# Kernel optimization log

Measured on AMD Instinct MI355X. Metric: run time of the kernel, lower is better.

## Reference

```python
import jax, jax.numpy as jnp
import numpy as np

MASK_ID = -100
L, D, HID, NH = 10, 768, 3072, 12
DH = D // NH
REACH = 2  # (sliding_window_size - 1) // 2 with window 5


def _layernorm(x, g, b, eps=1e-5):
    mu = x.mean(-1, keepdims=True)
    var = ((x - mu) ** 2).mean(-1, keepdims=True)
    return (x - mu) * jax.lax.rsqrt(var + eps) * g + b


def _adaln(x, temb, w, bb, g, be):
    # AdaLayerNormShiftScale: linear(silu(temb)) -> (scale, shift)
    e = jax.nn.silu(temb) @ w + bb
    scale, shift = jnp.split(e, 2, axis=-1)
    return _layernorm(x, g, be) * (1.0 + scale) + shift


def _timestep_emb(t):
    half = D // 2
    exponent = -np.log(10000.0) * jnp.arange(half, dtype=jnp.float32) / (half - 1.0)
    freq = jnp.exp(exponent)  # [half]
    emb = t.astype(jnp.float32)[..., None] * freq  # [b,s,half]
    return jnp.concatenate([jnp.sin(emb), jnp.cos(emb)], axis=-1)  # [b,s,D]


def setup_inputs():
    key = jax.random.key(0)
    ks = jax.random.split(key, 16)
    b, s = 4, 1024
    # packed token ids: 4 samples of 256 tokens (16x16 grid), last 64 tokens padding
    idx = np.arange(s)
    sid = idx // 256
    hpos = (idx % 256) // 16
    wpos = idx % 16
    sid = np.where(idx >= 960, MASK_ID, sid)
    tok = np.stack([sid, hpos, wpos], axis=-1)  # [s,3]
    token_ids = jnp.asarray(np.broadcast_to(tok, (b, s, 3)).copy(), dtype=jnp.int32)
    t = jax.random.randint(ks[0], (b, 1), 0, L + 1).astype(jnp.int32)
    t = jnp.broadcast_to(t, (b, s))

    def w(k, shape):
        return jax.random.normal(k, shape, jnp.float32) * 0.02

    return dict(
        x=jax.random.normal(ks[1], (b, s, D), jnp.float32),
        t=t,
        token_ids=token_ids,
        proj_in_w=w(ks[2], (D, D)), proj_in_b=jnp.zeros((D,), jnp.float32),
        h_emb=w(ks[3], (64, D)), w_emb=w(ks[4], (64, D)),
        adaln1_w=w(ks[5], (L, D, 2 * D)), adaln1_b=jnp.zeros((L, 2 * D), jnp.float32),
        ln1_g=jnp.ones((L, D), jnp.float32), ln1_b=jnp.zeros((L, D), jnp.float32),
        qkv_w=w(ks[6], (L, D, 3 * D)), qkv_b=jnp.zeros((L, 3 * D), jnp.float32),
        o_w=w(ks[7], (L, D, D)), o_b=jnp.zeros((L, D), jnp.float32),
        adaln2_w=w(ks[8], (L, D, 2 * D)), adaln2_b=jnp.zeros((L, 2 * D), jnp.float32),
        ln2_g=jnp.ones((L, D), jnp.float32), ln2_b=jnp.zeros((L, D), jnp.float32),
        fc1_w=w(ks[9], (L, D, HID)), fc1_b=jnp.zeros((L, HID), jnp.float32),
        fc2_w=w(ks[10], (L, HID, D)), fc2_b=jnp.zeros((L, D), jnp.float32),
        nout_w=w(ks[11], (D, 2 * D)), nout_b=jnp.zeros((2 * D,), jnp.float32),
        nout_g=jnp.ones((D,), jnp.float32), nout_beta=jnp.zeros((D,), jnp.float32),
    )


def _encoder(x, t, token_ids, proj_in_w, proj_in_b, h_emb, w_emb,
             adaln1_w, adaln1_b, ln1_g, ln1_b, qkv_w, qkv_b, o_w, o_b,
             adaln2_w, adaln2_b, ln2_g, ln2_b, fc1_w, fc1_b, fc2_w, fc2_b,
             nout_w, nout_b, nout_g, nout_beta):
    b, s, _ = x.shape
    sample_ids = token_ids[..., 0]          # [b,s]
    pos = token_ids[..., 1:]                # [b,s,2]
    x = x @ proj_in_w + proj_in_b
    x = x + h_emb[pos[..., 0]] + w_emb[pos[..., 1]]

    # block-sparse mask: same packed sample, Chebyshev sliding window, no padding queries
    same = sample_ids[:, :, None] == sample_ids[:, None, :]              # [b,s,s]
    cheby = jnp.abs(pos[:, :, None, :] - pos[:, None, :, :]).max(-1)      # [b,s,s]
    notpad_q = (sample_ids != MASK_ID)[:, :, None]
    mask = same & (cheby <= REACH) & notpad_q                             # [b,s,s]
    row_valid = mask.any(-1)[..., None]                                   # [b,s,1]

    temb = _timestep_emb(t)  # [b,s,D]
    scale = 1.0 / np.sqrt(DH)
    for i in range(L):
        h1 = _adaln(x, temb, adaln1_w[i], adaln1_b[i], ln1_g[i], ln1_b[i])
        qkv = h1 @ qkv_w[i] + qkv_b[i]
        q, k, v = jnp.split(qkv, 3, axis=-1)
        q = q.reshape(b, s, NH, DH)
        k = k.reshape(b, s, NH, DH)
        v = v.reshape(b, s, NH, DH)
        scores = jnp.einsum('bqhd,bkhd->bhqk', q, k) * scale
        scores = jnp.where(mask[:, None], scores, -1e30)
        attn = jax.nn.softmax(scores, axis=-1)
        o = jnp.einsum('bhqk,bkhd->bqhd', attn, v).reshape(b, s, D)
        o = jnp.where(row_valid, o, 0.0)  # fully-masked (padding) rows -> 0
        x = x + o @ o_w[i] + o_b[i]
        h2 = _adaln(x, temb, adaln2_w[i], adaln2_b[i], ln2_g[i], ln2_b[i])
        x = x + jax.nn.gelu(h2 @ fc1_w[i] + fc1_b[i], approximate=False) @ fc2_w[i] + fc2_b[i]
    x = _adaln(x, temb, nout_w, nout_b, nout_g, nout_beta)
    return x


def reference(x, t, token_ids, proj_in_w, proj_in_b, h_emb, w_emb,
              adaln1_w, adaln1_b, ln1_g, ln1_b, qkv_w, qkv_b, o_w, o_b,
              adaln2_w, adaln2_b, ln2_g, ln2_b, fc1_w, fc1_b, fc2_w, fc2_b,
              nout_w, nout_b, nout_g, nout_beta):
    return _encoder(x, t, token_ids, proj_in_w, proj_in_b, h_emb, w_emb,
                    adaln1_w, adaln1_b, ln1_g, ln1_b, qkv_w, qkv_b, o_w, o_b,
                    adaln2_w, adaln2_b, ln2_g, ln2_b, fc1_w, fc1_b, fc2_w, fc2_b,
                    nout_w, nout_b, nout_g, nout_beta)
```

## Files before the change

kernel.cpp:

```cpp
#include <hip/hip_runtime.h>
#include <hip/hip_bf16.h>
#include <math.h>

#define MASK_ID (-100)
#define SEQ 1024
#define BATCH 4
#define DMODEL 768
#define NHEAD 12
#define DHEAD 64
#define NLAYER 10
#define HIDDEN 3072

typedef unsigned short ushort_t;
typedef unsigned int uint_t;

__device__ __forceinline__ ushort_t f2bf(float f) {
    uint_t u = __float_as_uint(f);
    u = u + 0x7fffu + ((u >> 16) & 1u);
    return (ushort_t)(u >> 16);
}
__device__ __forceinline__ float bf2f(ushort_t u) {
    return __uint_as_float(((uint_t)u) << 16);
}

__device__ __forceinline__ void async_ld16(ushort_t* lds, const ushort_t* g) {
    __builtin_amdgcn_global_load_lds((__attribute__((address_space(1))) const void*)g,
                                     (__attribute__((address_space(3))) void*)lds, 16, 0, 0);
}

#define WAITVM(n) asm volatile("s_waitcnt vmcnt(" #n ")" ::: "memory")

__global__ void temb_silu_kernel(const int* __restrict__ t, float* __restrict__ stemb) {
    int b = blockIdx.x;
    int j = threadIdx.x;
    float tv = (float)t[b * SEQ];
    float freq = expf(-logf(10000.f) * (float)j / 383.f);
    float arg = tv * freq;
    float s = sinf(arg), c = cosf(arg);
    stemb[b * DMODEL + j]       = s / (1.f + expf(-s));
    stemb[b * DMODEL + 384 + j] = c / (1.f + expf(-c));
}

__global__ __launch_bounds__(256)
void adaln_partial_kernel(const float* __restrict__ stemb,
                          const float* __restrict__ a1w,
                          const float* __restrict__ a2w,
                          const float* __restrict__ nw,
                          float* __restrict__ partial) {
    int chunk = blockIdx.x;
    int kc    = blockIdx.y;
    int slot  = blockIdx.z;
    int tid = threadIdx.x;
    int col = chunk * 256 + tid;
    const float* W;
    if (slot == 20) W = nw;
    else {
        int i = slot >> 1;
        W = ((slot & 1) ? a2w : a1w) + (size_t)i * DMODEL * 2 * DMODEL;
    }
    __shared__ float sb[4 * 96];
    for (int idx = tid; idx < 4 * 96; idx += 256) {
        int bb = idx / 96, kk = idx % 96;
        sb[idx] = stemb[bb * DMODEL + kc * 96 + kk];
    }
    __syncthreads();
    const float* Wp = W + (size_t)(kc * 96) * (2 * DMODEL) + col;
    float a0 = 0.f, a1 = 0.f, a2 = 0.f, a3 = 0.f;
    #pragma unroll 4
    for (int kk = 0; kk < 96; ++kk) {
        float w = Wp[(size_t)kk * (2 * DMODEL)];
        a0 = fmaf(sb[kk], w, a0);
        a1 = fmaf(sb[96 + kk], w, a1);
        a2 = fmaf(sb[192 + kk], w, a2);
        a3 = fmaf(sb[288 + kk], w, a3);
    }
    size_t base = ((size_t)(slot * 8 + kc) * 4) * (2 * DMODEL) + col;
    partial[base + 0 * 2 * DMODEL] = a0;
    partial[base + 1 * 2 * DMODEL] = a1;
    partial[base + 2 * 2 * DMODEL] = a2;
    partial[base + 3 * 2 * DMODEL] = a3;
}

__global__ __launch_bounds__(256)
void adaln_reduce_kernel(const float* __restrict__ partial,
                         const float* __restrict__ a1b, const float* __restrict__ a2b,
                         const float* __restrict__ nb,
                         float* __restrict__ e_all) {
    int chunk = blockIdx.x;
    int slot  = blockIdx.y;
    int col = chunk * 256 + threadIdx.x;
    const float* bb;
    if (slot == 20) bb = nb;
    else {
        int i = slot >> 1;
        bb = ((slot & 1) ? a2b : a1b) + i * 2 * DMODEL;
    }
    float bias = bb[col];
    float s0 = bias, s1 = bias, s2 = bias, s3 = bias;
    #pragma unroll
    for (int kc = 0; kc < 8; ++kc) {
        size_t base = ((size_t)(slot * 8 + kc) * 4) * (2 * DMODEL) + col;
        s0 += partial[base + 0 * 2 * DMODEL];
        s1 += partial[base + 1 * 2 * DMODEL];
        s2 += partial[base + 2 * 2 * DMODEL];
        s3 += partial[base + 3 * 2 * DMODEL];
    }
    size_t o = (size_t)slot * 4 * (2 * DMODEL) + col;
    e_all[o + 0 * 2 * DMODEL] = s0;
    e_all[o + 1 * 2 * DMODEL] = s1;
    e_all[o + 2 * 2 * DMODEL] = s2;
    e_all[o + 3 * 2 * DMODEL] = s3;
}

__global__ __launch_bounds__(256)
void transpose_bf16_kernel(const float* __restrict__ in, ushort_t* __restrict__ out,
                           int R, int C) {
    __shared__ float tile[32][33];
    int tx = threadIdx.x & 31, ty = threadIdx.x >> 5;
    int c0 = blockIdx.x * 32, r0 = blockIdx.y * 32;
    #pragma unroll
    for (int i = 0; i < 4; ++i)
        tile[ty + 8 * i][tx] = in[(size_t)(r0 + ty + 8 * i) * C + c0 + tx];
    __syncthreads();
    #pragma unroll
    for (int i = 0; i < 4; ++i)
        out[(size_t)(c0 + ty + 8 * i) * R + r0 + tx] = f2bf(tile[tx][ty + 8 * i]);
}

__global__ __launch_bounds__(256)
void transpose_all_kernel(const float* __restrict__ w0, const float* __restrict__ w1,
                          const float* __restrict__ w2, const float* __restrict__ w3,
                          ushort_t* __restrict__ o0, ushort_t* __restrict__ o1,
                          ushort_t* __restrict__ o2, ushort_t* __restrict__ o3) {
    int layer = blockIdx.y;
    int id = blockIdx.x;
    const float* in; ushort_t* out; int R, C, tile_id, TX;
    if (id < 216) {
        in = w0 + (size_t)layer * DMODEL * 3 * DMODEL; out = o0 + (size_t)layer * 3 * DMODEL * DMODEL;
        R = DMODEL; C = 3 * DMODEL; tile_id = id; TX = 36;
    } else if (id < 288) {
        in = w1 + (size_t)layer * DMODEL * DMODEL; out = o1 + (size_t)layer * DMODEL * DMODEL;
        R = DMODEL; C = DMODEL; tile_id = id - 216; TX = 12;
    } else if (id < 576) {
        in = w2 + (size_t)layer * DMODEL * HIDDEN; out = o2 + (size_t)layer * HIDDEN * DMODEL;
        R = DMODEL; C = HIDDEN; tile_id = id - 288; TX = 48;
    } else {
        in = w3 + (size_t)layer * HIDDEN * DMODEL; out = o3 + (size_t)layer * DMODEL * HIDDEN;
        R = HIDDEN; C = DMODEL; tile_id = id - 576; TX = 12;
    }
    int c0 = (tile_id % TX) * 64, r0 = (tile_id / TX) * 128;
    __shared__ float tl[128][65];
    int tid = threadIdx.x;
    #pragma unroll
    for (int i = 0; i < 32; ++i) {
        int idx = i * 256 + tid;
        int r = idx >> 6, c = idx & 63;
        tl[r][c] = in[(size_t)(r0 + r) * C + c0 + c];
    }
    __syncthreads();
    #pragma unroll
    for (int j = 0; j < 16; ++j) {
        int idx = j * 256 + tid;
        int oc = idx >> 6, pr = idx & 63;
        float a = tl[pr * 2][oc], b = tl[pr * 2 + 1][oc];
        uint_t pk = (uint_t)f2bf(a) | ((uint_t)f2bf(b) << 16);
        *(uint_t*)&out[(size_t)(c0 + oc) * R + r0 + pr * 2] = pk;
    }
}

__global__ __launch_bounds__(256)
void f32_to_bf16_kernel(const float* __restrict__ in, ushort_t* __restrict__ out, int n8) {
    int i = blockIdx.x * 256 + threadIdx.x;
    if (i >= n8) return;
    float4 a = ((const float4*)in)[2 * i];
    float4 b = ((const float4*)in)[2 * i + 1];
    uint4 o;
    o.x = (uint_t)f2bf(a.x) | ((uint_t)f2bf(a.y) << 16);
    o.y = (uint_t)f2bf(a.z) | ((uint_t)f2bf(a.w) << 16);
    o.z = (uint_t)f2bf(b.x) | ((uint_t)f2bf(b.y) << 16);
    o.w = (uint_t)f2bf(b.z) | ((uint_t)f2bf(b.w) << 16);
    ((uint4*)out)[i] = o;
}

template<int OUT_BF>
__global__ __launch_bounds__(256)
void ln_adaln_kernel(const float* __restrict__ in, void* __restrict__ outv,
                     const float* __restrict__ g, const float* __restrict__ be,
                     const float* __restrict__ e) {
    int wid = threadIdx.x >> 6, lane = threadIdx.x & 63;
    int row = blockIdx.x * 4 + wid;
    int b = row >> 10;
    const float* xr = in + (size_t)row * DMODEL;
    float v[12];
    float s = 0.f, ss = 0.f;
    #pragma unroll
    for (int j = 0; j < 12; ++j) {
        v[j] = xr[lane + j * 64];
        s += v[j];
        ss = fmaf(v[j], v[j], ss);
    }
    #pragma unroll
    for (int o = 1; o < 64; o <<= 1) { s += __shfl_xor(s, o); ss += __shfl_xor(ss, o); }
    float mu = s * (1.f / DMODEL);
    float var = ss * (1.f / DMODEL) - mu * mu;
    float rs = rsqrtf(var + 1e-5f);
    const float* esc = e + (size_t)b * (2 * DMODEL);
    #pragma unroll
    for (int j = 0; j < 12; ++j) {
        int c = lane + j * 64;
        float y = (v[j] - mu) * rs * g[c] + be[c];
        y = y * (1.f + esc[c]) + esc[DMODEL + c];
        if (OUT_BF) ((ushort_t*)outv)[(size_t)row * DMODEL + c] = f2bf(y);
        else        ((float*)outv)[(size_t)row * DMODEL + c] = y;
    }
}

__device__ __forceinline__ float gelu_exact(float x) {
    return 0.5f * x * (1.f + erff(x * 0.70710678118654752f));
}

template<int BM, int BN, int EPI, int OCC>
__global__ __launch_bounds__(256, OCC)
void gemm_bf16(const ushort_t* __restrict__ A, const ushort_t* __restrict__ Wt,
               const float* __restrict__ bias, void* __restrict__ outv,
               const float* __restrict__ emb_h, const float* __restrict__ emb_w,
               const int* __restrict__ tok,
               int M, int N, int K) {
    constexpr int WM = BM / 2, WN = BN / 2;
    constexpr int FM = WM / 16, FN = WN / 16;
    constexpr int BUF = (BM + BN) * 64;
    constexpr int LPT = (BM + BN) / 32;
    using f32x4  = __attribute__((ext_vector_type(4))) float;
    using bf16x8 = __attribute__((ext_vector_type(8))) short;

    __shared__ __align__(16) ushort_t lds[3 * BUF];

    int tid = threadIdx.x;
    int lane = tid & 63, wid = tid >> 6;
    int wr = wid >> 1, wc = wid & 1;
    int l16 = lane & 15, lg = lane >> 4;
    int sw = l16 & 7;

    int nx = N / BN;
    int cpx = gridDim.x >> 3;
    int wg = blockIdx.x;
    int wgid = (wg & 7) * cpx + (wg >> 3);
    int bx = wgid % nx, by = wgid / nx;
    int bm0 = by * BM, bn0 = bx * BN;

    f32x4 acc[FM][FN];
    #pragma unroll
    for (int m = 0; m < FM; ++m)
        #pragma unroll
        for (int n = 0; n < FN; ++n)
            #pragma unroll
            for (int r = 0; r < 4; ++r) acc[m][n][r] = 0.f;

    const ushort_t* Abase = A + (size_t)bm0 * K;
    const ushort_t* Bbase = Wt + (size_t)bn0 * K;

    #define STAGE(bufi, kt)                                                             \
        do {                                                                            \
            _Pragma("unroll")                                                           \
            for (int s2 = 0; s2 < BM / 32; ++s2) {                                      \
                int ca = s2 * 256 + tid;                                                \
                int rw = ca >> 3, kcs = (ca & 7) ^ (rw & 7);                            \
                async_ld16(&lds[(bufi) * BUF + ca * 8],                                 \
                           Abase + (size_t)rw * K + (kt) * 64 + kcs * 8);               \
            }                                                                           \
            _Pragma("unroll")                                                           \
            for (int s2 = 0; s2 < BN / 32; ++s2) {                                      \
                int ca = s2 * 256 + tid;                                                \
                int rw = ca >> 3, kcs = (ca & 7) ^ (rw & 7);                            \
                async_ld16(&lds[(bufi) * BUF + BM * 64 + ca * 8],                       \
                           Bbase + (size_t)rw * K + (kt) * 64 + kcs * 8);               \
            }                                                                           \
        } while (0)

    int nk = K >> 6;
    STAGE(0, 0);
    STAGE(1, 1);
    int bufi = 0;
    for (int kt = 0; kt < nk; ++kt) {
        int nxt = bufi + 2; if (nxt >= 3) nxt -= 3;
        if (kt + 2 < nk) {
            STAGE(nxt, kt + 2);
            if constexpr (LPT == 4) WAITVM(8); else WAITVM(12);
        } else if (kt + 1 < nk) {
            if constexpr (LPT == 4) WAITVM(4); else WAITVM(6);
        } else {
            WAITVM(0);
        }
        __builtin_amdgcn_s_barrier();
        __builtin_amdgcn_s_setprio(1);
        #pragma unroll
        for (int kk = 0; kk < 2; ++kk) {
            bf16x8 af[FM], bfr[FN];
            #pragma unroll
            for (int m = 0; m < FM; ++m) {
                int row = wr * WM + m * 16 + l16;
                int csw = (kk * 4 + lg) ^ sw;
                af[m] = *(const bf16x8*)&lds[bufi * BUF + row * 64 + csw * 8];
            }
            #pragma unroll
            for (int n = 0; n < FN; ++n) {
                int row = wc * WN + n * 16 + l16;
                int csw = (kk * 4 + lg) ^ sw;
                bfr[n] = *(const bf16x8*)&lds[bufi * BUF + BM * 64 + row * 64 + csw * 8];
            }
            #pragma unroll
            for (int m = 0; m < FM; ++m)
                #pragma unroll
                for (int n = 0; n < FN; ++n)
                    acc[m][n] = __builtin_amdgcn_mfma_f32_16x16x32_bf16(af[m], bfr[n], acc[m][n], 0, 0, 0);
        }
        __builtin_amdgcn_s_setprio(0);
        __builtin_amdgcn_s_barrier();
        ++bufi; if (bufi >= 3) bufi = 0;
    }
    #undef STAGE

    int r0 = bm0 + wr * WM, c0 = bn0 + wc * WN;
    #pragma unroll
    for (int m = 0; m < FM; ++m) {
        #pragma unroll
        for (int n = 0; n < FN; ++n) {
            int cc = c0 + n * 16 + l16;
            float bcol = bias[cc];
            #pragma unroll
            for (int r = 0; r < 4; ++r) {
                int row = r0 + m * 16 + lg * 4 + r;
                float v = acc[m][n][r] + bcol;
                if (EPI == 0) {
                    ((ushort_t*)outv)[(size_t)row * N + cc] = f2bf(v);
                } else if (EPI == 1) {
                    int p0 = tok[row * 3 + 1], p1 = tok[row * 3 + 2];
                    v += emb_h[p0 * DMODEL + cc] + emb_w[p1 * DMODEL + cc];
                    ((float*)outv)[(size_t)row * N + cc] = v;
                } else if (EPI == 2) {
                    float* op = (float*)outv + (size_t)row * N + cc;
                    *op = *op + v;
                } else {
                    ((ushort_t*)outv)[(size_t)row * N + cc] = f2bf(gelu_exact(v));
                }
            }
        }
    }
}

__global__ __launch_bounds__(256)
void attn_kernel(const ushort_t* __restrict__ qkv, const int* __restrict__ tok,
                 ushort_t* __restrict__ o_out) {
    int tid = threadIdx.x;
    int u = tid >> 2, part = tid & 3;
    int q = blockIdx.x * 16 + (u & 15);
    int h = blockIdx.y * 4 + (u >> 4);
    int b = blockIdx.z;
    int m = b * SEQ + q;
    ushort_t* op = o_out + (size_t)m * DMODEL + h * DHEAD + part * 16;
    int sid = tok[m * 3];
    if (sid == MASK_ID) {
        uint4 z = {0u, 0u, 0u, 0u};
        ((uint4*)op)[0] = z;
        ((uint4*)op)[1] = z;
        return;
    }
    int qh = tok[m * 3 + 1], qw = tok[m * 3 + 2];
    const ushort_t* qp = qkv + (size_t)m * (3 * DMODEL) + h * DHEAD + part * 16;
    float qv[16], ov[16];
    {
        uint4 u0 = ((const uint4*)qp)[0];
        uint4 u1 = ((const uint4*)qp)[1];
        qv[0] = bf2f(u0.x & 0xffff); qv[1] = bf2f(u0.x >> 16);
        qv[2] = bf2f(u0.y & 0xffff); qv[3] = bf2f(u0.y >> 16);
        qv[4] = bf2f(u0.z & 0xffff); qv[5] = bf2f(u0.z >> 16);
        qv[6] = bf2f(u0.w & 0xffff); qv[7] = bf2f(u0.w >> 16);
        qv[8]  = bf2f(u1.x & 0xffff); qv[9]  = bf2f(u1.x >> 16);
        qv[10] = bf2f(u1.y & 0xffff); qv[11] = bf2f(u1.y >> 16);
        qv[12] = bf2f(u1.z & 0xffff); qv[13] = bf2f(u1.z >> 16);
        qv[14] = bf2f(u1.w & 0xffff); qv[15] = bf2f(u1.w >> 16);
    }
    #pragma unroll
    for (int i = 0; i < 16; ++i) ov[i] = 0.f;
    float mx = -1e30f, den = 0.f;
    for (int dh = -2; dh <= 2; ++dh) {
        for (int dw = -2; dw <= 2; ++dw) {
            int kq = q + dh * 16 + dw;
            if (kq < 0 || kq >= SEQ) continue;
            int km = b * SEQ + kq;
            if (tok[km * 3] != sid) continue;
            int kh2 = tok[km * 3 + 1], kw2 = tok[km * 3 + 2];
            int adh = kh2 - qh; if (adh < 0) adh = -adh;
            int adw = kw2 - qw; if (adw < 0) adw = -adw;
            if (adh > 2 || adw > 2) continue;
            const ushort_t* kp = qkv + (size_t)km * (3 * DMODEL) + DMODEL + h * DHEAD + part * 16;
            float dot;
            {
                uint4 u0 = ((const uint4*)kp)[0];
                uint4 u1 = ((const uint4*)kp)[1];
                dot = qv[0] * bf2f(u0.x & 0xffff);
                dot = fmaf(qv[1], bf2f(u0.x >> 16), dot);
                dot = fmaf(qv[2], bf2f(u0.y & 0xffff), dot);
                dot = fmaf(qv[3], bf2f(u0.y >> 16), dot);
                dot = fmaf(qv[4], bf2f(u0.z & 0xffff), dot);
                dot = fmaf(qv[5], bf2f(u0.z >> 16), dot);
                dot = fmaf(qv[6], bf2f(u0.w & 0xffff), dot);
                dot = fmaf(qv[7], bf2f(u0.w >> 16), dot);
                dot = fmaf(qv[8],  bf2f(u1.x & 0xffff), dot);
                dot = fmaf(qv[9],  bf2f(u1.x >> 16), dot);
                dot = fmaf(qv[10], bf2f(u1.y & 0xffff), dot);
                dot = fmaf(qv[11], bf2f(u1.y >> 16), dot);
                dot = fmaf(qv[12], bf2f(u1.z & 0xffff), dot);
                dot = fmaf(qv[13], bf2f(u1.z >> 16), dot);
                dot = fmaf(qv[14], bf2f(u1.w & 0xffff), dot);
                dot = fmaf(qv[15], bf2f(u1.w >> 16), dot);
            }
            dot += __shfl_xor(dot, 1);
            dot += __shfl_xor(dot, 2);
            float sc = dot * 0.125f;
            float nm = fmaxf(mx, sc);
            float c1 = expf(mx - nm);
            float c2 = expf(sc - nm);
            den = den * c1 + c2;
            const ushort_t* vp = qkv + (size_t)km * (3 * DMODEL) + 2 * DMODEL + h * DHEAD + part * 16;
            {
                uint4 u0 = ((const uint4*)vp)[0];
                uint4 u1 = ((const uint4*)vp)[1];
                ov[0] = ov[0] * c1 + c2 * bf2f(u0.x & 0xffff);
                ov[1] = ov[1] * c1 + c2 * bf2f(u0.x >> 16);
                ov[2] = ov[2] * c1 + c2 * bf2f(u0.y & 0xffff);
                ov[3] = ov[3] * c1 + c2 * bf2f(u0.y >> 16);
                ov[4] = ov[4] * c1 + c2 * bf2f(u0.z & 0xffff);
                ov[5] = ov[5] * c1 + c2 * bf2f(u0.z >> 16);
                ov[6] = ov[6] * c1 + c2 * bf2f(u0.w & 0xffff);
                ov[7] = ov[7] * c1 + c2 * bf2f(u0.w >> 16);
                ov[8]  = ov[8]  * c1 + c2 * bf2f(u1.x & 0xffff);
                ov[9]  = ov[9]  * c1 + c2 * bf2f(u1.x >> 16);
                ov[10] = ov[10] * c1 + c2 * bf2f(u1.y & 0xffff);
                ov[11] = ov[11] * c1 + c2 * bf2f(u1.y >> 16);
                ov[12] = ov[12] * c1 + c2 * bf2f(u1.z & 0xffff);
                ov[13] = ov[13] * c1 + c2 * bf2f(u1.z >> 16);
                ov[14] = ov[14] * c1 + c2 * bf2f(u1.w & 0xffff);
                ov[15] = ov[15] * c1 + c2 * bf2f(u1.w >> 16);
            }
            mx = nm;
        }
    }
    float inv = 1.f / den;
    uint4 o0, o1;
    o0.x = (uint_t)f2bf(ov[0] * inv) | ((uint_t)f2bf(ov[1] * inv) << 16);
    o0.y = (uint_t)f2bf(ov[2] * inv) | ((uint_t)f2bf(ov[3] * inv) << 16);
    o0.z = (uint_t)f2bf(ov[4] * inv) | ((uint_t)f2bf(ov[5] * inv) << 16);
    o0.w = (uint_t)f2bf(ov[6] * inv) | ((uint_t)f2bf(ov[7] * inv) << 16);
    o1.x = (uint_t)f2bf(ov[8]  * inv) | ((uint_t)f2bf(ov[9]  * inv) << 16);
    o1.y = (uint_t)f2bf(ov[10] * inv) | ((uint_t)f2bf(ov[11] * inv) << 16);
    o1.z = (uint_t)f2bf(ov[12] * inv) | ((uint_t)f2bf(ov[13] * inv) << 16);
    o1.w = (uint_t)f2bf(ov[14] * inv) | ((uint_t)f2bf(ov[15] * inv) << 16);
    ((uint4*)op)[0] = o0;
    ((uint4*)op)[1] = o1;
}

extern "C" void kernel_launch(void* const* d_in, const int* in_sizes, int n_in,
                              void* d_out, int out_size, void* d_ws, size_t ws_size,
                              hipStream_t stream) {
    const float* x_in      = (const float*)d_in[0];
    const int*   t         = (const int*)d_in[1];
    const int*   tok       = (const int*)d_in[2];
    const float* proj_in_w = (const float*)d_in[3];
    const float* proj_in_b = (const float*)d_in[4];
    const float* h_emb     = (const float*)d_in[5];
    const float* w_emb     = (const float*)d_in[6];
    const float* adaln1_w  = (const float*)d_in[7];
    const float* adaln1_b  = (const float*)d_in[8];
    const float* ln1_g     = (const float*)d_in[9];
    const float* ln1_b     = (const float*)d_in[10];
    const float* qkv_w     = (const float*)d_in[11];
    const float* qkv_b     = (const float*)d_in[12];
    const float* o_w       = (const float*)d_in[13];
    const float* o_b       = (const float*)d_in[14];
    const float* adaln2_w  = (const float*)d_in[15];
    const float* adaln2_b  = (const float*)d_in[16];
    const float* ln2_g     = (const float*)d_in[17];
    const float* ln2_b     = (const float*)d_in[18];
    const float* fc1_w     = (const float*)d_in[19];
    const float* fc1_b     = (const float*)d_in[20];
    const float* fc2_w     = (const float*)d_in[21];
    const float* fc2_b     = (const float*)d_in[22];
    const float* nout_w    = (const float*)d_in[23];
    const float* nout_b    = (const float*)d_in[24];
    const float* nout_g    = (const float*)d_in[25];
    const float* nout_beta = (const float*)d_in[26];

    const int M = BATCH * SEQ;

    float* stemb   = (float*)d_ws;
    float* e_all   = stemb + BATCH * DMODEL;
    float* partial = e_all + 21 * BATCH * 2 * DMODEL;
    ushort_t* h_bf   = (ushort_t*)(partial + 21 * 8 * 4 * 2 * DMODEL);
    ushort_t* qkv_bf = h_bf + (size_t)M * DMODEL;
    ushort_t* hid_bf = qkv_bf + (size_t)M * 3 * DMODEL;
    ushort_t* projT  = hid_bf + (size_t)M * HIDDEN;
    ushort_t* qkvT_a = projT + (size_t)DMODEL * DMODEL;
    ushort_t* oT_a   = qkvT_a + (size_t)NLAYER * 3 * DMODEL * DMODEL;
    ushort_t* fc1T_a = oT_a + (size_t)NLAYER * DMODEL * DMODEL;
    ushort_t* fc2T_a = fc1T_a + (size_t)NLAYER * DMODEL * HIDDEN;
    float* x = (float*)d_out;

    temb_silu_kernel<<<BATCH, 384, 0, stream>>>(t, stemb);
    adaln_partial_kernel<<<dim3(6, 8, 2 * NLAYER + 1), 256, 0, stream>>>(
        stemb, adaln1_w, adaln2_w, nout_w, partial);
    adaln_reduce_kernel<<<dim3(6, 2 * NLAYER + 1), 256, 0, stream>>>(
        partial, adaln1_b, adaln2_b, nout_b, e_all);

    transpose_all_kernel<<<dim3(864, NLAYER), 256, 0, stream>>>(
        qkv_w, o_w, fc1_w, fc2_w, qkvT_a, oT_a, fc1T_a, fc2T_a);
    transpose_bf16_kernel<<<dim3(DMODEL / 32, DMODEL / 32), 256, 0, stream>>>(proj_in_w, projT, DMODEL, DMODEL);

    f32_to_bf16_kernel<<<(M * DMODEL / 8 + 255) / 256, 256, 0, stream>>>(x_in, h_bf, M * DMODEL / 8);
    gemm_bf16<64, 64, 1, 3><<<(DMODEL / 64) * (M / 64), 256, 0, stream>>>(
        h_bf, projT, proj_in_b, x, h_emb, w_emb, tok, M, DMODEL, DMODEL);

    for (int i = 0; i < NLAYER; ++i) {
        ln_adaln_kernel<1><<<M / 4, 256, 0, stream>>>(
            x, h_bf, ln1_g + i * DMODEL, ln1_b + i * DMODEL,
            e_all + (size_t)(2 * i) * BATCH * 2 * DMODEL);
        gemm_bf16<64, 128, 0, 2><<<(3 * DMODEL / 128) * (M / 64), 256, 0, stream>>>(
            h_bf, qkvT_a + (size_t)i * 3 * DMODEL * DMODEL, qkv_b + i * 3 * DMODEL,
            qkv_bf, nullptr, nullptr, nullptr, M, 3 * DMODEL, DMODEL);
        attn_kernel<<<dim3(SEQ / 16, NHEAD / 4, BATCH), 256, 0, stream>>>(qkv_bf, tok, h_bf);
        gemm_bf16<64, 64, 2, 3><<<(DMODEL / 64) * (M / 64), 256, 0, stream>>>(
            h_bf, oT_a + (size_t)i * DMODEL * DMODEL, o_b + i * DMODEL,
            x, nullptr, nullptr, nullptr, M, DMODEL, DMODEL);
        ln_adaln_kernel<1><<<M / 4, 256, 0, stream>>>(
            x, h_bf, ln2_g + i * DMODEL, ln2_b + i * DMODEL,
            e_all + (size_t)(2 * i + 1) * BATCH * 2 * DMODEL);
        gemm_bf16<64, 128, 3, 2><<<(HIDDEN / 128) * (M / 64), 256, 0, stream>>>(
            h_bf, fc1T_a + (size_t)i * DMODEL * HIDDEN, fc1_b + i * HIDDEN,
            hid_bf, nullptr, nullptr, nullptr, M, HIDDEN, DMODEL);
        gemm_bf16<64, 64, 2, 3><<<(DMODEL / 64) * (M / 64), 256, 0, stream>>>(
            hid_bf, fc2T_a + (size_t)i * DMODEL * HIDDEN, fc2_b + i * DMODEL,
            x, nullptr, nullptr, nullptr, M, DMODEL, HIDDEN);
    }

    ln_adaln_kernel<0><<<M / 4, 256, 0, stream>>>(
        x, x, nout_g, nout_beta, e_all + (size_t)(2 * NLAYER) * BATCH * 2 * DMODEL);
}
```

Baseline: 1.839 ms.

## Use larger single-buffered GEMM tiles and a bf16-staged weight transpose

The GEMM drops its three-stage async LDS pipeline in favour of a single buffer with a full wait and barrier each k-step, and moves to larger 128-row tiles, which halves the grid and raises the occupancy hint. The weight transpose now uses 64x64 tiles, loads float4 and converts to bf16 before storing to shared memory, with twice as many blocks. Larger tiles are meant to improve operand reuse and cut the number of blocks. The price is that load latency is no longer hidden behind MFMA work, and the small N=768 GEMMs get fewer blocks to spread across the CUs.

```diff
diff --git a/kernel.cpp b/kernel.cpp
--- a/kernel.cpp
+++ b/kernel.cpp
@@ -135,35 +135,38 @@
     int layer = blockIdx.y;
     int id = blockIdx.x;
     const float* in; ushort_t* out; int R, C, tile_id, TX;
-    if (id < 216) {
+    if (id < 432) {
         in = w0 + (size_t)layer * DMODEL * 3 * DMODEL; out = o0 + (size_t)layer * 3 * DMODEL * DMODEL;
         R = DMODEL; C = 3 * DMODEL; tile_id = id; TX = 36;
-    } else if (id < 288) {
+    } else if (id < 576) {
         in = w1 + (size_t)layer * DMODEL * DMODEL; out = o1 + (size_t)layer * DMODEL * DMODEL;
-        R = DMODEL; C = DMODEL; tile_id = id - 216; TX = 12;
-    } else if (id < 576) {
+        R = DMODEL; C = DMODEL; tile_id = id - 432; TX = 12;
+    } else if (id < 1152) {
         in = w2 + (size_t)layer * DMODEL * HIDDEN; out = o2 + (size_t)layer * HIDDEN * DMODEL;
-        R = DMODEL; C = HIDDEN; tile_id = id - 288; TX = 48;
+        R = DMODEL; C = HIDDEN; tile_id = id - 576; TX = 48;
     } else {
         in = w3 + (size_t)layer * HIDDEN * DMODEL; out = o3 + (size_t)layer * DMODEL * HIDDEN;
-        R = HIDDEN; C = DMODEL; tile_id = id - 576; TX = 12;
-    }
-    int c0 = (tile_id % TX) * 64, r0 = (tile_id / TX) * 128;
-    __shared__ float tl[128][65];
+        R = HIDDEN; C = DMODEL; tile_id = id - 1152; TX = 12;
+    }
+    int c0 = (tile_id % TX) * 64, r0 = (tile_id / TX) * 64;
+    __shared__ ushort_t tlb[64 * 65];
     int tid = threadIdx.x;
     #pragma unroll
-    for (int i = 0; i < 32; ++i) {
+    for (int i = 0; i < 4; ++i) {
         int idx = i * 256 + tid;
-        int r = idx >> 6, c = idx & 63;
-        tl[r][c] = in[(size_t)(r0 + r) * C + c0 + c];
+        int r = idx >> 4, c4 = (idx & 15) * 4;
+        float4 v = *(const float4*)&in[(size_t)(r0 + r) * C + c0 + c4];
+        tlb[r * 65 + c4 + 0] = f2bf(v.x);
+        tlb[r * 65 + c4 + 1] = f2bf(v.y);
+        tlb[r * 65 + c4 + 2] = f2bf(v.z);
+        tlb[r * 65 + c4 + 3] = f2bf(v.w);
     }
     __syncthreads();
     #pragma unroll
-    for (int j = 0; j < 16; ++j) {
+    for (int j = 0; j < 8; ++j) {
         int idx = j * 256 + tid;
-        int oc = idx >> 6, pr = idx & 63;
-        float a = tl[pr * 2][oc], b = tl[pr * 2 + 1][oc];
-        uint_t pk = (uint_t)f2bf(a) | ((uint_t)f2bf(b) << 16);
+        int oc = idx >> 5, pr = idx & 31;
+        uint_t pk = (uint_t)tlb[(pr * 2) * 65 + oc] | ((uint_t)tlb[(pr * 2 + 1) * 65 + oc] << 16);
         *(uint_t*)&out[(size_t)(c0 + oc) * R + r0 + pr * 2] = pk;
     }
 }
@@ -221,19 +224,17 @@
 
 template<int BM, int BN, int EPI, int OCC>
 __global__ __launch_bounds__(256, OCC)
-void gemm_bf16(const ushort_t* __restrict__ A, const ushort_t* __restrict__ Wt,
-               const float* __restrict__ bias, void* __restrict__ outv,
-               const float* __restrict__ emb_h, const float* __restrict__ emb_w,
-               const int* __restrict__ tok,
-               int M, int N, int K) {
+void gemm_big(const ushort_t* __restrict__ A, const ushort_t* __restrict__ Wt,
+              const float* __restrict__ bias, void* __restrict__ outv,
+              const float* __restrict__ emb_h, const float* __restrict__ emb_w,
+              const int* __restrict__ tok,
+              int M, int N, int K) {
     constexpr int WM = BM / 2, WN = BN / 2;
     constexpr int FM = WM / 16, FN = WN / 16;
-    constexpr int BUF = (BM + BN) * 64;
-    constexpr int LPT = (BM + BN) / 32;
     using f32x4  = __attribute__((ext_vector_type(4))) float;
     using bf16x8 = __attribute__((ext_vector_type(8))) short;
 
-    __shared__ __align__(16) ushort_t lds[3 * BUF];
+    __shared__ __align__(16) ushort_t lds[(BM + BN) * 64];
 
     int tid = threadIdx.x;
     int lane = tid & 63, wid = tid >> 6;
@@ -259,66 +260,40 @@
     const ushort_t* Abase = A + (size_t)bm0 * K;
     const ushort_t* Bbase = Wt + (size_t)bn0 * K;
 
-    #define STAGE(bufi, kt)                                                             \
-        do {                                                                            \
-            _Pragma("unroll")                                                           \
-            for (int s2 = 0; s2 < BM / 32; ++s2) {                                      \
-                int ca = s2 * 256 + tid;                                                \
-                int rw = ca >> 3, kcs = (ca & 7) ^ (rw & 7);                            \
-                async_ld16(&lds[(bufi) * BUF + ca * 8],                                 \
-                           Abase + (size_t)rw * K + (kt) * 64 + kcs * 8);               \
-            }                                                                           \
-            _Pragma("unroll")                                                           \
-            for (int s2 = 0; s2 < BN / 32; ++s2) {                                      \
-                int ca = s2 * 256 + tid;                                                \
-                int rw = ca >> 3, kcs = (ca & 7) ^ (rw & 7);                            \
-                async_ld16(&lds[(bufi) * BUF + BM * 64 + ca * 8],                       \
-                           Bbase + (size_t)rw * K + (kt) * 64 + kcs * 8);               \
-            }                                                                           \
-        } while (0)
-
     int nk = K >> 6;
-    STAGE(0, 0);
-    STAGE(1, 1);
-    int bufi = 0;
     for (int kt = 0; kt < nk; ++kt) {
-        int nxt = bufi + 2; if (nxt >= 3) nxt -= 3;
-        if (kt + 2 < nk) {
-            STAGE(nxt, kt + 2);
-            if constexpr (LPT == 4) WAITVM(8); else WAITVM(12);
-        } else if (kt + 1 < nk) {
-            if constexpr (LPT == 4) WAITVM(4); else WAITVM(6);
-        } else {
-            WAITVM(0);
+        #pragma unroll
+        for (int s2 = 0; s2 < BM / 32; ++s2) {
+            int ca = s2 * 256 + tid;
+            int rw = ca >> 3, kcs = (ca & 7) ^ (rw & 7);
+            async_ld16(&lds[ca * 8], Abase + (size_t)rw * K + kt * 64 + kcs * 8);
         }
-        __builtin_amdgcn_s_barrier();
-        __builtin_amdgcn_s_setprio(1);
+        #pragma unroll
+        for (int s2 = 0; s2 < BN / 32; ++s2) {
+            int ca = s2 * 256 + tid;
+            int rw = ca >> 3, kcs = (ca & 7) ^ (rw & 7);
+            async_ld16(&lds[BM * 64 + ca * 8], Bbase + (size_t)rw * K + kt * 64 + kcs * 8);
+        }
+        WAITVM(0);
+        __syncthreads();
         #pragma unroll
         for (int kk = 0; kk < 2; ++kk) {
+            int csw = (kk * 4 + lg) ^ sw;
             bf16x8 af[FM], bfr[FN];
             #pragma unroll
-            for (int m = 0; m < FM; ++m) {
-                int row = wr * WM + m * 16 + l16;
-                int csw = (kk * 4 + lg) ^ sw;
-                af[m] = *(const bf16x8*)&lds[bufi * BUF + row * 64 + csw * 8];
-            }
+            for (int m = 0; m < FM; ++m)
+                af[m] = *(const bf16x8*)&lds[(wr * WM + m * 16 + l16) * 64 + csw * 8];
             #pragma unroll
-            for (int n = 0; n < FN; ++n) {
-                int row = wc * WN + n * 16 + l16;
-                int csw = (kk * 4 + lg) ^ sw;
-                bfr[n] = *(const bf16x8*)&lds[bufi * BUF + BM * 64 + row * 64 + csw * 8];
-            }
+            for (int n = 0; n < FN; ++n)
+                bfr[n] = *(const bf16x8*)&lds[BM * 64 + (wc * WN + n * 16 + l16) * 64 + csw * 8];
             #pragma unroll
             for (int m = 0; m < FM; ++m)
                 #pragma unroll
                 for (int n = 0; n < FN; ++n)
                     acc[m][n] = __builtin_amdgcn_mfma_f32_16x16x32_bf16(af[m], bfr[n], acc[m][n], 0, 0, 0);
         }
-        __builtin_amdgcn_s_setprio(0);
-        __builtin_amdgcn_s_barrier();
-        ++bufi; if (bufi >= 3) bufi = 0;
-    }
-    #undef STAGE
+        __syncthreads();
+    }
 
     int r0 = bm0 + wr * WM, c0 = bn0 + wc * WN;
     #pragma unroll
@@ -512,32 +487,32 @@
     adaln_reduce_kernel<<<dim3(6, 2 * NLAYER + 1), 256, 0, stream>>>(
         partial, adaln1_b, adaln2_b, nout_b, e_all);
 
-    transpose_all_kernel<<<dim3(864, NLAYER), 256, 0, stream>>>(
+    transpose_all_kernel<<<dim3(1728, NLAYER), 256, 0, stream>>>(
         qkv_w, o_w, fc1_w, fc2_w, qkvT_a, oT_a, fc1T_a, fc2T_a);
     transpose_bf16_kernel<<<dim3(DMODEL / 32, DMODEL / 32), 256, 0, stream>>>(proj_in_w, projT, DMODEL, DMODEL);
 
     f32_to_bf16_kernel<<<(M * DMODEL / 8 + 255) / 256, 256, 0, stream>>>(x_in, h_bf, M * DMODEL / 8);
-    gemm_bf16<64, 64, 1, 3><<<(DMODEL / 64) * (M / 64), 256, 0, stream>>>(
+    gemm_big<128, 64, 1, 4><<<(DMODEL / 64) * (M / 128), 256, 0, stream>>>(
         h_bf, projT, proj_in_b, x, h_emb, w_emb, tok, M, DMODEL, DMODEL);
 
     for (int i = 0; i < NLAYER; ++i) {
         ln_adaln_kernel<1><<<M / 4, 256, 0, stream>>>(
             x, h_bf, ln1_g + i * DMODEL, ln1_b + i * DMODEL,
             e_all + (size_t)(2 * i) * BATCH * 2 * DMODEL);
-        gemm_bf16<64, 128, 0, 2><<<(3 * DMODEL / 128) * (M / 64), 256, 0, stream>>>(
+        gemm_big<128, 128, 0, 3><<<(3 * DMODEL / 128) * (M / 128), 256, 0, stream>>>(
             h_bf, qkvT_a + (size_t)i * 3 * DMODEL * DMODEL, qkv_b + i * 3 * DMODEL,
             qkv_bf, nullptr, nullptr, nullptr, M, 3 * DMODEL, DMODEL);
         attn_kernel<<<dim3(SEQ / 16, NHEAD / 4, BATCH), 256, 0, stream>>>(qkv_bf, tok, h_bf);
-        gemm_bf16<64, 64, 2, 3><<<(DMODEL / 64) * (M / 64), 256, 0, stream>>>(
+        gemm_big<128, 64, 2, 4><<<(DMODEL / 64) * (M / 128), 256, 0, stream>>>(
             h_bf, oT_a + (size_t)i * DMODEL * DMODEL, o_b + i * DMODEL,
             x, nullptr, nullptr, nullptr, M, DMODEL, DMODEL);
         ln_adaln_kernel<1><<<M / 4, 256, 0, stream>>>(
             x, h_bf, ln2_g + i * DMODEL, ln2_b + i * DMODEL,
             e_all + (size_t)(2 * i + 1) * BATCH * 2 * DMODEL);
-        gemm_bf16<64, 128, 3, 2><<<(HIDDEN / 128) * (M / 64), 256, 0, stream>>>(
+        gemm_big<128, 128, 3, 3><<<(HIDDEN / 128) * (M / 128), 256, 0, stream>>>(
             h_bf, fc1T_a + (size_t)i * DMODEL * HIDDEN, fc1_b + i * HIDDEN,
             hid_bf, nullptr, nullptr, nullptr, M, HIDDEN, DMODEL);
-        gemm_bf16<64, 64, 2, 3><<<(DMODEL / 64) * (M / 64), 256, 0, stream>>>(
+        gemm_big<128, 64, 2, 4><<<(DMODEL / 64) * (M / 128), 256, 0, stream>>>(
             hid_bf, fc2T_a + (size_t)i * DMODEL * HIDDEN, fc2_b + i * DMODEL,
             x, nullptr, nullptr, nullptr, M, DMODEL, HIDDEN);
     }
```

Result: slower. 1.923 ms (+4.6%).
